# Kernel tuning notes

Measured on AMD Instinct MI355X. Metric: run time of the kernel, lower is better.

Reference implementation:

```python
import jax, jax.numpy as jnp
import numpy as np

B, F, D, E = 16384, 2048, 256, 8  # batch, feature, expert out dim, n instrument experts (+1 default)


def setup_inputs() -> dict:
    key = jax.random.key(0)
    k1, k2, k3 = jax.random.split(key, 3)
    shared_features = jax.random.normal(k1, (B, F), dtype=jnp.float32)
    # instrument ids 0..E-1; id_to_index is the identity mapping here
    instrument_ids = jax.random.randint(k2, (B, 1), 0, E, dtype=jnp.int32)
    # stacked expert weights: E instrument layers + 1 default layer => E+1 Dense(F->D)
    W = jax.random.normal(k3, (E + 1, F, D), dtype=jnp.float32) * 0.02
    b = jnp.zeros((E + 1, D), dtype=jnp.float32)
    return {"shared_features": shared_features, "W": W, "b": b,
            "instrument_ids": instrument_ids}


def reference(shared_features, W, b, instrument_ids):
    # Compute ALL expert projections on the full batch (faithful to the TF layer),
    # stacked on axis=1: [B, E+1, D]
    stacked = jnp.einsum('bf,efd->bed', shared_features, W) + b
    # id_to_index lookup: ids are 0..E-1, identity mapping; default layer at index E unused
    idx = instrument_ids[:, 0].astype(jnp.int32)  # [B]
    # gather_nd equivalent: select per-sample expert output -> [B, D]
    selected = jnp.take_along_axis(stacked, idx[:, None, None], axis=1)[:, 0, :]
    return selected
```

## Files before the change

### kernel.cpp

```cpp
#include <hip/hip_runtime.h>
#include <hip/hip_bf16.h>

#define B_SZ 16384
#define F_SZ 2048
#define D_SZ 256
#define E_SZ 8
#define GRID_G 528

typedef __attribute__((ext_vector_type(8))) short bhalf8;
typedef __attribute__((ext_vector_type(4))) float fl4;

__device__ __forceinline__ short f2b(float f) {
  __hip_bfloat16 h = __float2bfloat16(f);
  union { __hip_bfloat16 h; short s; } u;
  u.h = h;
  return u.s;
}

__global__ void k_scatter(const int* __restrict__ ids, int* __restrict__ counts,
                          int* __restrict__ perm) {
  __shared__ int lcnt[E_SZ], lbase[E_SZ];
  int t = threadIdx.x;
  if (t < E_SZ) lcnt[t] = 0;
  __syncthreads();
  int b = blockIdx.x * 256 + t;
  int e = ids[b];
  int p = atomicAdd(&lcnt[e], 1);
  __syncthreads();
  if (t < E_SZ) lbase[t] = atomicAdd(&counts[t], lcnt[t]);
  __syncthreads();
  perm[e * B_SZ + lbase[e] + p] = b;
}

__global__ void k_transpose(const float* __restrict__ W, __hip_bfloat16* __restrict__ Wt) {
  __shared__ float tile[64][65];
  int e = blockIdx.z;
  int f0 = blockIdx.x * 64;
  int d0 = blockIdx.y * 64;
  int t = threadIdx.x;
  const float* src = W + ((size_t)e * F_SZ + f0) * D_SZ + d0;
  int fr = t >> 2, c0 = t & 3;
#pragma unroll
  for (int c = c0; c < 16; c += 4) {
    float4 v = *(const float4*)(src + (size_t)fr * D_SZ + c * 4);
    tile[fr][c * 4 + 0] = v.x;
    tile[fr][c * 4 + 1] = v.y;
    tile[fr][c * 4 + 2] = v.z;
    tile[fr][c * 4 + 3] = v.w;
  }
  __syncthreads();
  int dr = t >> 2, cc = t & 3;
  union { unsigned short u[16]; bhalf8 v[2]; } pk;
#pragma unroll
  for (int k = 0; k < 16; ++k) pk.u[k] = (unsigned short)f2b(tile[cc * 16 + k][dr]);
  __hip_bfloat16* dst = Wt + ((size_t)e * D_SZ + d0 + dr) * F_SZ + f0 + cc * 16;
  ((bhalf8*)dst)[0] = pk.v[0];
  ((bhalf8*)dst)[1] = pk.v[1];
}

__device__ __forceinline__ void load_lds16(const __hip_bfloat16* g, __hip_bfloat16* l) {
  __builtin_amdgcn_global_load_lds((const __attribute__((address_space(1))) void*)g,
                                   (__attribute__((address_space(3))) void*)l, 16, 0, 0);
}

__launch_bounds__(512, 4)
__global__ void k_gemm(const float* __restrict__ x, const __hip_bfloat16* __restrict__ Wt,
                       const float* __restrict__ bias, const int* __restrict__ counts,
                       const int* __restrict__ perm, float* __restrict__ out) {
  int id = blockIdx.x;
  int nb = (id & 1) * 128;
  int mt = id >> 1;
  int e = -1, mbase = 0, count = 0;
  {
    int acc0 = 0;
#pragma unroll
    for (int ee = 0; ee < E_SZ; ++ee) {
      int c = counts[ee];
      int nt = (c + 63) >> 6;
      if (e < 0 && mt < acc0 + nt) { e = ee; mbase = (mt - acc0) * 64; count = c; }
      acc0 += nt;
    }
  }
  if (e < 0) return;

  __shared__ __align__(16) __hip_bfloat16 As[2 * 64 * 64];
  __shared__ __align__(16) __hip_bfloat16 Bs[2 * 128 * 64];

  int t = threadIdx.x;
  int w = t >> 6;
  int lane = t & 63;
  int wm = w >> 2, wn = w & 3;
  int l15 = lane & 15;
  int q = lane >> 4;

  const int* permE = perm + e * B_SZ;

  int tr = t >> 4;
  int tc = t & 15;
  const float* pA[2];
  int wAo[2];
#pragma unroll
  for (int i = 0; i < 2; ++i) {
    int r = i * 32 + tr;
    int gm = mbase + r;
    int src = permE[(gm < count) ? gm : mbase];
    pA[i] = x + (size_t)src * F_SZ + tc * 4;
    int cw = tc >> 1, half = tc & 1;
    wAo[i] = r * 64 + ((cw ^ (r & 7)) * 8) + half * 4;
  }

  const __hip_bfloat16* pB[2];
  int dB[2];
#pragma unroll
  for (int i = 0; i < 2; ++i) {
    int p = i * 512 + t;
    int n = p >> 3;
    int cl = (p & 7) ^ (n & 7);
    pB[i] = Wt + (size_t)(e * D_SZ + nb + n) * F_SZ + cl * 8;
    dB[i] = i * 4096 + w * 512;
  }

  int rAo[2][2], rBo[2][2];
#pragma unroll
  for (int ks = 0; ks < 2; ++ks) {
#pragma unroll
    for (int i = 0; i < 2; ++i) {
      int m = wm * 32 + i * 16 + l15;
      rAo[ks][i] = m * 64 + (((ks * 4 + q) ^ (m & 7)) * 8);
    }
#pragma unroll
    for (int j = 0; j < 2; ++j) {
      int n = wn * 32 + j * 16 + l15;
      rBo[ks][j] = n * 64 + (((ks * 4 + q) ^ (n & 7)) * 8);
    }
  }

  fl4 zz = {0.0f, 0.0f, 0.0f, 0.0f};
  fl4 acc[2][2];
#pragma unroll
  for (int i = 0; i < 2; ++i)
#pragma unroll
    for (int j = 0; j < 2; ++j) acc[i][j] = zz;

  float4 av[2];

#pragma unroll
  for (int i = 0; i < 2; ++i) load_lds16(pB[i], Bs + dB[i]);
  __builtin_amdgcn_sched_barrier(0);
#pragma unroll
  for (int i = 0; i < 2; ++i) av[i] = *(const float4*)(pA[i]);
#pragma unroll
  for (int i = 0; i < 2; ++i) {
    short4 s;
    s.x = f2b(av[i].x); s.y = f2b(av[i].y);
    s.z = f2b(av[i].z); s.w = f2b(av[i].w);
    *(short4*)(As + wAo[i]) = s;
  }
#pragma unroll
  for (int i = 0; i < 2; ++i) av[i] = *(const float4*)(pA[i] + 64);
  __builtin_amdgcn_sched_barrier(0);
  asm volatile("s_waitcnt vmcnt(2) lgkmcnt(0)");
  __builtin_amdgcn_sched_barrier(0);
  __builtin_amdgcn_s_barrier();
  __builtin_amdgcn_sched_barrier(0);

  for (int k = 0; k < 31; ++k) {
    int cb = (k & 1);
    int nx = cb ^ 1;
#pragma unroll
    for (int i = 0; i < 2; ++i) load_lds16(pB[i] + (k + 1) * 64, Bs + nx * 8192 + dB[i]);
    __builtin_amdgcn_sched_barrier(0);
#pragma unroll
    for (int i = 0; i < 2; ++i) {
      short4 s;
      s.x = f2b(av[i].x); s.y = f2b(av[i].y);
      s.z = f2b(av[i].z); s.w = f2b(av[i].w);
      *(short4*)(As + nx * 4096 + wAo[i]) = s;
    }
    int kn = (k + 2) & 31;
#pragma unroll
    for (int i = 0; i < 2; ++i) av[i] = *(const float4*)(pA[i] + kn * 64);
    {
      const __hip_bfloat16* Ab = As + cb * 4096;
      const __hip_bfloat16* Bb = Bs + cb * 8192;
#pragma unroll
      for (int ks = 0; ks < 2; ++ks) {
        bhalf8 af[2], bf[2];
#pragma unroll
        for (int i = 0; i < 2; ++i) af[i] = *(const bhalf8*)(Ab + rAo[ks][i]);
#pragma unroll
        for (int j = 0; j < 2; ++j) bf[j] = *(const bhalf8*)(Bb + rBo[ks][j]);
#pragma unroll
        for (int i = 0; i < 2; ++i)
#pragma unroll
          for (int j = 0; j < 2; ++j)
            acc[i][j] = __builtin_amdgcn_mfma_f32_16x16x32_bf16(af[i], bf[j], acc[i][j], 0, 0, 0);
      }
    }
    __builtin_amdgcn_sched_barrier(0);
    asm volatile("s_waitcnt vmcnt(2) lgkmcnt(0)");
    __builtin_amdgcn_sched_barrier(0);
    __builtin_amdgcn_s_barrier();
    __builtin_amdgcn_sched_barrier(0);
  }
  asm volatile("" :: "v"(av[0].x), "v"(av[1].x));

  {
    const __hip_bfloat16* Ab = As + 4096;
    const __hip_bfloat16* Bb = Bs + 8192;
#pragma unroll
    for (int ks = 0; ks < 2; ++ks) {
      bhalf8 af[2], bf[2];
#pragma unroll
      for (int i = 0; i < 2; ++i) af[i] = *(const bhalf8*)(Ab + rAo[ks][i]);
#pragma unroll
      for (int j = 0; j < 2; ++j) bf[j] = *(const bhalf8*)(Bb + rBo[ks][j]);
#pragma unroll
      for (int i = 0; i < 2; ++i)
#pragma unroll
        for (int j = 0; j < 2; ++j)
          acc[i][j] = __builtin_amdgcn_mfma_f32_16x16x32_bf16(af[i], bf[j], acc[i][j], 0, 0, 0);
    }
  }

  float bv[2];
#pragma unroll
  for (int j = 0; j < 2; ++j) bv[j] = bias[e * D_SZ + nb + wn * 32 + j * 16 + l15];

#pragma unroll
  for (int i = 0; i < 2; ++i) {
#pragma unroll
    for (int r = 0; r < 4; ++r) {
      int gm = mbase + wm * 32 + i * 16 + q * 4 + r;
      if (gm < count) {
        int row = permE[gm];
        float* po = out + (size_t)row * D_SZ + nb + wn * 32;
#pragma unroll
        for (int j = 0; j < 2; ++j) po[j * 16 + l15] = acc[i][j][r] + bv[j];
      }
    }
  }
}

extern "C" void kernel_launch(void* const* d_in, const int* in_sizes, int n_in,
                              void* d_out, int out_size, void* d_ws, size_t ws_size,
                              hipStream_t stream) {
  const float* x = (const float*)d_in[0];
  const float* W = (const float*)d_in[1];
  const float* bias = (const float*)d_in[2];
  const int* ids = (const int*)d_in[3];
  float* out = (float*)d_out;

  char* ws = (char*)d_ws;
  int* counts = (int*)ws;
  int* perm = (int*)(ws + 256);
  __hip_bfloat16* Wt = (__hip_bfloat16*)(ws + (1 << 20));

  hipMemsetAsync(counts, 0, E_SZ * sizeof(int), stream);
  k_scatter<<<B_SZ / 256, 256, 0, stream>>>(ids, counts, perm);
  k_transpose<<<dim3(F_SZ / 64, D_SZ / 64, E_SZ), 256, 0, stream>>>(W, Wt);
  k_gemm<<<GRID_G, 512, 0, stream>>>(x, Wt, bias, counts, perm, out);
}
```

Before: 253.0 us.

## Deepen A-tile register prefetch and remap block ids across XCDs

Each thread now keeps two register sets for the fp32 A rows. The loop is unrolled by two so the global loads for activations are issued three k-steps ahead instead of two, hiding more gather latency. Separately, block ids are permuted so consecutive logical tiles, which share the same expert's weights, land on the same XCD for better L2 reuse. The cost is extra VGPRs for the second prefetch buffer. The in-loop vmcnt(2) wait still drains the previous iteration's loads, which may limit how much of the deeper prefetch is actually exploited.

```diff
diff --git a/kernel.cpp b/kernel.cpp
--- a/kernel.cpp
+++ b/kernel.cpp
@@ -6,6 +6,7 @@
 #define D_SZ 256
 #define E_SZ 8
 #define GRID_G 528
+#define XCHUNK (GRID_G / 8)
 
 typedef __attribute__((ext_vector_type(8))) short bhalf8;
 typedef __attribute__((ext_vector_type(4))) float fl4;
@@ -67,7 +68,8 @@
 __global__ void k_gemm(const float* __restrict__ x, const __hip_bfloat16* __restrict__ Wt,
                        const float* __restrict__ bias, const int* __restrict__ counts,
                        const int* __restrict__ perm, float* __restrict__ out) {
-  int id = blockIdx.x;
+  int bid = blockIdx.x;
+  int id = (bid & 7) * XCHUNK + (bid >> 3);
   int nb = (id & 1) * 128;
   int mt = id >> 1;
   int e = -1, mbase = 0, count = 0;
@@ -142,68 +144,85 @@
 #pragma unroll
     for (int j = 0; j < 2; ++j) acc[i][j] = zz;
 
-  float4 av[2];
+  float4 avA[2], avB[2];
 
 #pragma unroll
   for (int i = 0; i < 2; ++i) load_lds16(pB[i], Bs + dB[i]);
   __builtin_amdgcn_sched_barrier(0);
-#pragma unroll
-  for (int i = 0; i < 2; ++i) av[i] = *(const float4*)(pA[i]);
-#pragma unroll
-  for (int i = 0; i < 2; ++i) {
-    short4 s;
-    s.x = f2b(av[i].x); s.y = f2b(av[i].y);
-    s.z = f2b(av[i].z); s.w = f2b(av[i].w);
-    *(short4*)(As + wAo[i]) = s;
-  }
-#pragma unroll
-  for (int i = 0; i < 2; ++i) av[i] = *(const float4*)(pA[i] + 64);
-  __builtin_amdgcn_sched_barrier(0);
-  asm volatile("s_waitcnt vmcnt(2) lgkmcnt(0)");
-  __builtin_amdgcn_sched_barrier(0);
-  __builtin_amdgcn_s_barrier();
-  __builtin_amdgcn_sched_barrier(0);
-
-  for (int k = 0; k < 31; ++k) {
-    int cb = (k & 1);
-    int nx = cb ^ 1;
-#pragma unroll
-    for (int i = 0; i < 2; ++i) load_lds16(pB[i] + (k + 1) * 64, Bs + nx * 8192 + dB[i]);
-    __builtin_amdgcn_sched_barrier(0);
+  {
+    float4 avP[2];
+#pragma unroll
+    for (int i = 0; i < 2; ++i) avP[i] = *(const float4*)(pA[i]);
 #pragma unroll
     for (int i = 0; i < 2; ++i) {
       short4 s;
-      s.x = f2b(av[i].x); s.y = f2b(av[i].y);
-      s.z = f2b(av[i].z); s.w = f2b(av[i].w);
-      *(short4*)(As + nx * 4096 + wAo[i]) = s;
-    }
-    int kn = (k + 2) & 31;
-#pragma unroll
-    for (int i = 0; i < 2; ++i) av[i] = *(const float4*)(pA[i] + kn * 64);
-    {
-      const __hip_bfloat16* Ab = As + cb * 4096;
-      const __hip_bfloat16* Bb = Bs + cb * 8192;
-#pragma unroll
-      for (int ks = 0; ks < 2; ++ks) {
-        bhalf8 af[2], bf[2];
-#pragma unroll
-        for (int i = 0; i < 2; ++i) af[i] = *(const bhalf8*)(Ab + rAo[ks][i]);
-#pragma unroll
-        for (int j = 0; j < 2; ++j) bf[j] = *(const bhalf8*)(Bb + rBo[ks][j]);
-#pragma unroll
-        for (int i = 0; i < 2; ++i)
-#pragma unroll
-          for (int j = 0; j < 2; ++j)
-            acc[i][j] = __builtin_amdgcn_mfma_f32_16x16x32_bf16(af[i], bf[j], acc[i][j], 0, 0, 0);
-      }
-    }
-    __builtin_amdgcn_sched_barrier(0);
-    asm volatile("s_waitcnt vmcnt(2) lgkmcnt(0)");
-    __builtin_amdgcn_sched_barrier(0);
-    __builtin_amdgcn_s_barrier();
-    __builtin_amdgcn_sched_barrier(0);
-  }
-  asm volatile("" :: "v"(av[0].x), "v"(av[1].x));
+      s.x = f2b(avP[i].x); s.y = f2b(avP[i].y);
+      s.z = f2b(avP[i].z); s.w = f2b(avP[i].w);
+      *(short4*)(As + wAo[i]) = s;
+    }
+  }
+#pragma unroll
+  for (int i = 0; i < 2; ++i) avA[i] = *(const float4*)(pA[i] + 64);
+#pragma unroll
+  for (int i = 0; i < 2; ++i) avB[i] = *(const float4*)(pA[i] + 128);
+  __builtin_amdgcn_sched_barrier(0);
+  asm volatile("s_waitcnt vmcnt(4) lgkmcnt(0)");
+  __builtin_amdgcn_sched_barrier(0);
+  __builtin_amdgcn_s_barrier();
+  __builtin_amdgcn_sched_barrier(0);
+
+#define ITER(kk, AV)                                                                  \
+  do {                                                                                \
+    int cb_ = (kk) & 1, nx_ = cb_ ^ 1;                                                \
+    _Pragma("unroll")                                                                 \
+    for (int i = 0; i < 2; ++i)                                                       \
+      load_lds16(pB[i] + ((kk) + 1) * 64, Bs + nx_ * 8192 + dB[i]);                   \
+    __builtin_amdgcn_sched_barrier(0);                                                \
+    _Pragma("unroll")                                                                 \
+    for (int i = 0; i < 2; ++i) {                                                     \
+      short4 s;                                                                       \
+      s.x = f2b(AV[i].x); s.y = f2b(AV[i].y);                                         \
+      s.z = f2b(AV[i].z); s.w = f2b(AV[i].w);                                         \
+      *(short4*)(As + nx_ * 4096 + wAo[i]) = s;                                       \
+    }                                                                                 \
+    {                                                                                 \
+      int kn_ = ((kk) + 3) & 31;                                                      \
+      _Pragma("unroll")                                                               \
+      for (int i = 0; i < 2; ++i) AV[i] = *(const float4*)(pA[i] + kn_ * 64);         \
+    }                                                                                 \
+    {                                                                                 \
+      const __hip_bfloat16* Ab_ = As + cb_ * 4096;                                    \
+      const __hip_bfloat16* Bb_ = Bs + cb_ * 8192;                                    \
+      _Pragma("unroll")                                                               \
+      for (int ks = 0; ks < 2; ++ks) {                                                \
+        bhalf8 af[2], bf[2];                                                          \
+        _Pragma("unroll")                                                             \
+        for (int i = 0; i < 2; ++i) af[i] = *(const bhalf8*)(Ab_ + rAo[ks][i]);       \
+        _Pragma("unroll")                                                             \
+        for (int j = 0; j < 2; ++j) bf[j] = *(const bhalf8*)(Bb_ + rBo[ks][j]);       \
+        _Pragma("unroll")                                                             \
+        for (int i = 0; i < 2; ++i)                                                   \
+          _Pragma("unroll")                                                           \
+          for (int j = 0; j < 2; ++j)                                                 \
+            acc[i][j] = __builtin_amdgcn_mfma_f32_16x16x32_bf16(af[i], bf[j],         \
+                                                                acc[i][j], 0, 0, 0); \
+      }                                                                               \
+    }                                                                                 \
+    __builtin_amdgcn_sched_barrier(0);                                                \
+    asm volatile("s_waitcnt vmcnt(2) lgkmcnt(0)");                                    \
+    __builtin_amdgcn_sched_barrier(0);                                                \
+    __builtin_amdgcn_s_barrier();                                                     \
+    __builtin_amdgcn_sched_barrier(0);                                                \
+  } while (0)
+
+  for (int k = 0; k < 30; k += 2) {
+    ITER(k, avA);
+    ITER(k + 1, avB);
+  }
+  ITER(30, avA);
+#undef ITER
+
+  asm volatile("" :: "v"(avA[0].x), "v"(avA[1].x), "v"(avB[0].x), "v"(avB[1].x));
 
   {
     const __hip_bfloat16* Ab = As + 4096;
```

New measurement: 255.7 us. Within noise of the previous version (+1.0%).
